# Kernel tuning notes

Measured on AMD Instinct MI355X. Metric: run time of the kernel, lower is better.

## Reference

```python
import jax, jax.numpy as jnp
import numpy as np

B, T, C, H = 2, 2048, 1024, 16
HD = C // H          # head_dim = 64
HALF = HD // 2       # rope half dim = 32
ROPE_BASE = 10000.0


def _build_sin_cos(seq_len, half_dim, base=ROPE_BASE):
    # mirrors build_sin_cos: angles[t, i] = t * base^(-2i / (2*half_dim))
    pos = jnp.arange(seq_len, dtype=jnp.float32)[:, None]                     # [T,1]
    inv_freq = 1.0 / (base ** (jnp.arange(0, half_dim * 2, 2, dtype=jnp.float32) / (half_dim * 2)))
    angles = pos * inv_freq                                                   # [T, half]
    return jnp.sin(angles), jnp.cos(angles)


def setup_inputs() -> dict:
    key = jax.random.key(0)
    k1, k2, k3 = jax.random.split(key, 3)
    x = jax.random.normal(k1, (B, T, C), dtype=jnp.float32)
    # nn.Linear weights (stored as [out,in] in torch; we keep [in,out] for x @ W)
    Wqkv = jax.random.normal(k2, (C, 3 * C), dtype=jnp.float32) * (C ** -0.5)
    Wproj = jax.random.normal(k3, (C, C), dtype=jnp.float32) * (C ** -0.5)
    rope_sin, rope_cos = _build_sin_cos(T, HALF)
    return {"x": x, "Wqkv": Wqkv, "Wproj": Wproj, "rope_sin": rope_sin, "rope_cos": rope_cos}


def reference(x, Wqkv, Wproj, rope_sin, rope_cos):
    Bb, Tt, Cc = x.shape
    Hh = H
    hd = Cc // Hh
    # fused QKV projection, then per-head split (matches view(B,T,H,3*hd).split)
    qkv = (x @ Wqkv).reshape(Bb, Tt, Hh, 3 * hd)
    q, k, v = jnp.split(qkv, 3, axis=-1)                                      # each [B,T,H,hd]
    # RoPE (single device path: local slice == full range)
    s = rope_sin[:Tt][None, :, None, :].astype(x.dtype)                       # [1,T,1,half]
    c = rope_cos[:Tt][None, :, None, :].astype(x.dtype)

    def rot(t):
        t1, t2 = jnp.split(t, 2, axis=-1)
        return jnp.concatenate([t1 * c - t2 * s, t1 * s + t2 * c], axis=-1)

    q = rot(q)
    k = rot(k)
    # causal scaled dot-product attention (flash_attn default scale = hd^-0.5)
    scale = jnp.asarray(hd, x.dtype) ** -0.5
    scores = jnp.einsum('bqhd,bkhd->bhqk', q, k) * scale                      # [B,H,T,T]
    causal = jnp.tril(jnp.ones((Tt, Tt), dtype=bool))
    scores = jnp.where(causal, scores, jnp.finfo(x.dtype).min)
    probs = jax.nn.softmax(scores, axis=-1)
    attn = jnp.einsum('bhqk,bkhd->bqhd', probs, v).reshape(Bb, Tt, Cc)
    return attn @ Wproj
```

## Files before the change

### kernel.cpp

```cpp
#include <hip/hip_runtime.h>

#define Bb 2
#define Tt 2048
#define Cc_ 1024
#define Hh 16
#define HDd 64

typedef __attribute__((ext_vector_type(8))) short bf16x8;
typedef __attribute__((ext_vector_type(4))) float f32x4;
typedef __attribute__((ext_vector_type(4))) unsigned short u16x4;

__device__ __forceinline__ unsigned short f2bf(float f) {
  union { float f; unsigned int u; } v; v.f = f;
  unsigned int r = v.u + 0x7FFFu + ((v.u >> 16) & 1u);
  return (unsigned short)(r >> 16);
}
__device__ __forceinline__ float bf2f(unsigned short u) {
  union { unsigned int u; float f; } v; v.u = ((unsigned int)u) << 16;
  return v.f;
}
__device__ __forceinline__ f32x4 mfma16(bf16x8 a, bf16x8 b, f32x4 c) {
  return __builtin_amdgcn_mfma_f32_16x16x32_bf16(a, b, c, 0, 0, 0);
}
__device__ __forceinline__ void gl_lds16(const void* g, void* l) {
  auto* gp = reinterpret_cast<const __attribute__((address_space(1))) unsigned int*>(
      reinterpret_cast<unsigned long long>(g));
  auto* lp = reinterpret_cast<__attribute__((address_space(3))) unsigned int*>(
      reinterpret_cast<unsigned long long>(l));
  __builtin_amdgcn_global_load_lds(gp, lp, 16, 0, 0);
}

__global__ __launch_bounds__(256) void k_cvt(const float* __restrict__ in,
                                             unsigned short* __restrict__ out, int n4) {
  const int i = blockIdx.x * 256 + threadIdx.x;
  if (i >= n4) return;
  f32x4 v = ((const f32x4*)in)[i];
  u16x4 o;
  o[0] = f2bf(v[0]); o[1] = f2bf(v[1]); o[2] = f2bf(v[2]); o[3] = f2bf(v[3]);
  ((u16x4*)out)[i] = o;
}

__global__ __launch_bounds__(256) void k_tcvt(const float* __restrict__ in,
                                              unsigned short* __restrict__ out, int R, int Cc) {
  __shared__ float tile[32][33];
  const int c0 = blockIdx.x * 32, r0 = blockIdx.y * 32;
  const int tx = threadIdx.x, ty = threadIdx.y;
#pragma unroll
  for (int i = 0; i < 4; ++i)
    tile[ty + i * 8][tx] = in[(size_t)(r0 + ty + i * 8) * Cc + c0 + tx];
  __syncthreads();
#pragma unroll
  for (int i = 0; i < 4; ++i)
    out[(size_t)(c0 + ty + i * 8) * R + r0 + tx] = f2bf(tile[tx][ty + i * 8]);
}

template <bool OUT_BF16>
__global__ __launch_bounds__(256) void k_gemm(const unsigned short* __restrict__ A,
                                              const unsigned short* __restrict__ Bt,
                                              void* __restrict__ Cout, int M, int N, int K) {
  __shared__ unsigned short lA[128 * 64];
  __shared__ unsigned short lB[128 * 64];
  const int tid = threadIdx.x;
  const int lane = tid & 63, wid = tid >> 6;
  const int wr = wid >> 1, wc = wid & 1;
  const int bm = blockIdx.y * 128, bn = blockIdx.x * 128;
  const int l15 = lane & 15, l4 = lane >> 4;
  f32x4 acc[4][4];
#pragma unroll
  for (int i = 0; i < 4; ++i)
#pragma unroll
    for (int j = 0; j < 4; ++j) acc[i][j] = f32x4{0.f, 0.f, 0.f, 0.f};
  const int nk = K >> 6;
  for (int t = 0; t < nk; ++t) {
    const int k0 = t << 6;
    __syncthreads();
#pragma unroll
    for (int i = 0; i < 4; ++i) {
      const int slot = i * 256 + tid;
      const int row = slot >> 3, g = slot & 7;
      const int gs = (g ^ (row & 7)) * 8;
      gl_lds16(A + (size_t)(bm + row) * K + k0 + gs, &lA[slot * 8]);
      gl_lds16(Bt + (size_t)(bn + row) * K + k0 + gs, &lB[slot * 8]);
    }
    __syncthreads();
#pragma unroll
    for (int ks = 0; ks < 2; ++ks) {
      bf16x8 af[4], bfr[4];
#pragma unroll
      for (int mf = 0; mf < 4; ++mf) {
        const int row = wr * 64 + mf * 16 + l15;
        const int g = ks * 4 + l4;
        af[mf] = *(const bf16x8*)&lA[row * 64 + ((g ^ (row & 7)) * 8)];
      }
#pragma unroll
      for (int nf = 0; nf < 4; ++nf) {
        const int row = wc * 64 + nf * 16 + l15;
        const int g = ks * 4 + l4;
        bfr[nf] = *(const bf16x8*)&lB[row * 64 + ((g ^ (row & 7)) * 8)];
      }
#pragma unroll
      for (int mf = 0; mf < 4; ++mf)
#pragma unroll
        for (int nf = 0; nf < 4; ++nf)
          acc[mf][nf] = mfma16(af[mf], bfr[nf], acc[mf][nf]);
    }
  }
  const int rb = bm + wr * 64 + l4 * 4;
  const int cb = bn + wc * 64 + l15;
#pragma unroll
  for (int mf = 0; mf < 4; ++mf)
#pragma unroll
    for (int nf = 0; nf < 4; ++nf)
#pragma unroll
      for (int j = 0; j < 4; ++j) {
        const size_t idx = (size_t)(rb + mf * 16 + j) * N + cb + nf * 16;
        if (OUT_BF16)
          ((unsigned short*)Cout)[idx] = f2bf(acc[mf][nf][j]);
        else
          ((float*)Cout)[idx] = acc[mf][nf][j];
      }
}

__global__ __launch_bounds__(256) void k_rope(const unsigned short* __restrict__ qkv,
                                              const float* __restrict__ rsin,
                                              const float* __restrict__ rcos,
                                              unsigned short* __restrict__ Q,
                                              unsigned short* __restrict__ K) {
  const int tid = blockIdx.x * 256 + threadIdx.x;
  const int d = tid & 31;
  const int t = (tid >> 5) & 2047;
  const int h = (tid >> 16) & 15;
  const int b = tid >> 20;
  const size_t rq = (size_t)(b * Tt + t) * 3072 + h * 192;
  const float q1 = bf2f(qkv[rq + d]), q2 = bf2f(qkv[rq + 32 + d]);
  const float k1 = bf2f(qkv[rq + 64 + d]), k2 = bf2f(qkv[rq + 96 + d]);
  const float s = rsin[t * 32 + d], c = rcos[t * 32 + d];
  const size_t ob = ((size_t)(b * Hh + h) * Tt + t) * 64 + d;
  Q[ob] = f2bf((q1 * c - q2 * s) * 0.125f);
  Q[ob + 32] = f2bf((q1 * s + q2 * c) * 0.125f);
  K[ob] = f2bf(k1 * c - k2 * s);
  K[ob + 32] = f2bf(k1 * s + k2 * c);
}

__global__ __launch_bounds__(256) void k_vrep(const unsigned short* __restrict__ qkv,
                                              unsigned short* __restrict__ Vt) {
  __shared__ unsigned short tile[32][72];
  const int bh = blockIdx.y;
  const int t0 = blockIdx.x * 32;
  const int tx = threadIdx.x, ty = threadIdx.y;
  const int b = bh >> 4, h = bh & 15;
#pragma unroll
  for (int i = 0; i < 4; ++i) {
    const int trow = ty + i * 8;
    const size_t r = (size_t)(b * Tt + t0 + trow) * 3072 + h * 192 + 128;
    tile[trow][tx] = qkv[r + tx];
    tile[trow][tx + 32] = qkv[r + 32 + tx];
  }
  __syncthreads();
#pragma unroll
  for (int i = 0; i < 8; ++i) {
    const int d = ty + i * 8;
    Vt[((size_t)bh * 64 + d) * Tt + t0 + tx] = tile[tx][d];
  }
}

__global__ __launch_bounds__(256) void k_attn(const unsigned short* __restrict__ Q,
                                              const unsigned short* __restrict__ Kt,
                                              const unsigned short* __restrict__ Vt,
                                              unsigned short* __restrict__ Aout) {
  __shared__ unsigned short lK[64 * 64];
  __shared__ unsigned short lV[64 * 64];
  __shared__ unsigned short lP[4][16 * 64];
  const int bxq = blockIdx.x, bh = blockIdx.y;
  const int b = bh >> 4, h = bh & 15;
  const int tid = threadIdx.x, lane = tid & 63, w = tid >> 6;
  const int l15 = lane & 15, l4 = lane >> 4;
  const unsigned short* Kbh = Kt + (size_t)bh * Tt * 64;
  const unsigned short* Vbh = Vt + (size_t)bh * 64 * Tt;
  unsigned short* lPw = lP[w];
  for (int ph = 0; ph < 2; ++ph) {
    const int qt = ph ? bxq : (31 - bxq);
    const int qb = qt * 64;
    const size_t qoff = ((size_t)bh * Tt + qb + w * 16 + l15) * 64 + l4 * 8;
    const bf16x8 qf0 = *(const bf16x8*)&Q[qoff];
    const bf16x8 qf1 = *(const bf16x8*)&Q[qoff + 32];
    f32x4 o[4];
#pragma unroll
    for (int i = 0; i < 4; ++i) o[i] = f32x4{0.f, 0.f, 0.f, 0.f};
    float mrun = -1e30f, lrun = 0.f;
    const int nt = qt + 1;
    for (int t = 0; t < nt; ++t) {
      const int kv0 = t * 64;
      __syncthreads();
#pragma unroll
      for (int i = 0; i < 2; ++i) {
        const int slot = i * 256 + tid;
        const int row = slot >> 3, g = slot & 7;
        const int gs = (g ^ (row & 7)) * 8;
        gl_lds16(Kbh + (size_t)(kv0 + row) * 64 + gs, &lK[slot * 8]);
        gl_lds16(Vbh + (size_t)row * Tt + kv0 + gs, &lV[slot * 8]);
      }
      __syncthreads();
      f32x4 s[4];
#pragma unroll
      for (int i = 0; i < 4; ++i) s[i] = f32x4{0.f, 0.f, 0.f, 0.f};
      __builtin_amdgcn_s_setprio(1);
#pragma unroll
      for (int ks = 0; ks < 2; ++ks) {
        const bf16x8 qa = ks ? qf1 : qf0;
#pragma unroll
        for (int nf = 0; nf < 4; ++nf) {
          const int row = nf * 16 + l15;
          const int g = ks * 4 + l4;
          const bf16x8 kf = *(const bf16x8*)&lK[row * 64 + ((g ^ (row & 7)) * 8)];
          s[nf] = mfma16(kf, qa, s[nf]);
        }
      }
      __builtin_amdgcn_s_setprio(0);
      if (kv0 == qb) {
#pragma unroll
        for (int nf = 0; nf < 4; ++nf)
#pragma unroll
          for (int j = 0; j < 4; ++j)
            if (nf * 16 + l4 * 4 + j > w * 16 + l15) s[nf][j] = -3e38f;
      }
      float mx = s[0][0];
#pragma unroll
      for (int nf = 0; nf < 4; ++nf)
#pragma unroll
        for (int j = 0; j < 4; ++j)
          if (nf | j) mx = fmaxf(mx, s[nf][j]);
      mx = fmaxf(mx, __shfl_xor(mx, 16, 64));
      mx = fmaxf(mx, __shfl_xor(mx, 32, 64));
      const bool need = !__all(mx - mrun <= 8.0f);
      float mnew = mrun;
      if (need) mnew = fmaxf(mrun, mx);
      float ssum = 0.f;
#pragma unroll
      for (int nf = 0; nf < 4; ++nf) {
        u16x4 pk;
#pragma unroll
        for (int j = 0; j < 4; ++j) {
          const float p = __expf(s[nf][j] - mnew);
          ssum += p;
          pk[j] = f2bf(p);
        }
        const int g0 = nf * 2 + (l4 >> 1);
        *(u16x4*)&lPw[l15 * 64 + ((g0 ^ (l15 & 7)) * 8) + (l4 & 1) * 4] = pk;
      }
      ssum += __shfl_xor(ssum, 16, 64);
      ssum += __shfl_xor(ssum, 32, 64);
      if (need) {
        const float alpha = __expf(mrun - mnew);
        lrun = lrun * alpha + ssum;
        mrun = mnew;
        float aj[4];
#pragma unroll
        for (int j = 0; j < 4; ++j) aj[j] = __shfl(alpha, l4 * 4 + j, 64);
#pragma unroll
        for (int df = 0; df < 4; ++df)
#pragma unroll
          for (int j = 0; j < 4; ++j) o[df][j] *= aj[j];
      } else {
        lrun += ssum;
      }
      __builtin_amdgcn_s_setprio(1);
#pragma unroll
      for (int kb = 0; kb < 2; ++kb) {
        const bf16x8 pa = *(const bf16x8*)&lPw[l15 * 64 + (((kb * 4 + l4) ^ (l15 & 7)) * 8)];
#pragma unroll
        for (int df = 0; df < 4; ++df) {
          const int row = df * 16 + l15;
          const int g = kb * 4 + l4;
          const bf16x8 vb = *(const bf16x8*)&lV[row * 64 + ((g ^ (row & 7)) * 8)];
          o[df] = mfma16(pa, vb, o[df]);
        }
      }
      __builtin_amdgcn_s_setprio(0);
    }
    const float rinv = 1.f / lrun;
    float lj[4];
#pragma unroll
    for (int j = 0; j < 4; ++j) lj[j] = __shfl(rinv, l4 * 4 + j, 64);
#pragma unroll
    for (int j = 0; j < 4; ++j) {
      const size_t rr = (size_t)(b * Tt + qb + w * 16 + l4 * 4 + j) * 1024 + h * 64 + l15;
#pragma unroll
      for (int df = 0; df < 4; ++df) Aout[rr + df * 16] = f2bf(o[df][j] * lj[j]);
    }
  }
}

extern "C" void kernel_launch(void* const* d_in, const int* in_sizes, int n_in,
                              void* d_out, int out_size, void* d_ws, size_t ws_size,
                              hipStream_t stream) {
  const float* x = (const float*)d_in[0];
  const float* Wqkv = (const float*)d_in[1];
  const float* Wproj = (const float*)d_in[2];
  const float* rsin = (const float*)d_in[3];
  const float* rcos = (const float*)d_in[4];
  float* out = (float*)d_out;
  char* ws = (char*)d_ws;
  unsigned short* xb = (unsigned short*)(ws);
  unsigned short* wqkvt = (unsigned short*)(ws + (size_t)(8 << 20));
  unsigned short* wprot = (unsigned short*)(ws + (size_t)(14 << 20));
  unsigned short* qkv = (unsigned short*)(ws + (size_t)(16 << 20));
  unsigned short* Q = (unsigned short*)(ws + (size_t)(40 << 20));
  unsigned short* K = (unsigned short*)(ws + (size_t)(48 << 20));
  unsigned short* Vt = (unsigned short*)(ws + (size_t)(56 << 20));
  unsigned short* attn = (unsigned short*)(ws + (size_t)(64 << 20));

  k_cvt<<<4096, 256, 0, stream>>>(x, xb, 1048576);
  k_tcvt<<<dim3(96, 32), dim3(32, 8), 0, stream>>>(Wqkv, wqkvt, 1024, 3072);
  k_tcvt<<<dim3(32, 32), dim3(32, 8), 0, stream>>>(Wproj, wprot, 1024, 1024);
  k_gemm<true><<<dim3(24, 32), 256, 0, stream>>>(xb, wqkvt, qkv, 4096, 3072, 1024);
  k_rope<<<8192, 256, 0, stream>>>(qkv, rsin, rcos, Q, K);
  k_vrep<<<dim3(64, 32), dim3(32, 8), 0, stream>>>(qkv, Vt);
  k_attn<<<dim3(16, 32), 256, 0, stream>>>(Q, K, Vt, attn);
  k_gemm<false><<<dim3(8, 32), 256, 0, stream>>>(attn, wprot, out, 4096, 1024, 1024);
}
```

Baseline: 202.8 us.

## Double-buffer attention KV tiles, shrink query tile, add smaller-tile projection GEMM

Attention now uses 32-row query tiles with 128-thread blocks and twice as many blocks. K/V tiles are double-buffered in LDS so the next tile's global loads overlap the current tile's compute. Softmax moves to exp2 by folding log2(e) into the Q scale, and the max reduction becomes a balanced tree. The output projection switches to a new 128x64-tile GEMM that launches more blocks. The cost is more LDS per block, and smaller tiles mean more K/V reloads per query.

Result: no change. 205.3 us (+1.2%).

```diff
diff --git a/kernel.cpp b/kernel.cpp
--- a/kernel.cpp
+++ b/kernel.cpp
@@ -119,6 +119,72 @@
         else
           ((float*)Cout)[idx] = acc[mf][nf][j];
       }
+}
+
+__global__ __launch_bounds__(256) void k_gemm64(const unsigned short* __restrict__ A,
+                                                const unsigned short* __restrict__ Bt,
+                                                float* __restrict__ Cout, int M, int N, int K) {
+  __shared__ unsigned short lA[128 * 64];
+  __shared__ unsigned short lB[64 * 64];
+  const int tid = threadIdx.x;
+  const int lane = tid & 63, w = tid >> 6;
+  const int bm = blockIdx.y * 128, bn = blockIdx.x * 64;
+  const int l15 = lane & 15, l4 = lane >> 4;
+  f32x4 acc[2][4];
+#pragma unroll
+  for (int i = 0; i < 2; ++i)
+#pragma unroll
+    for (int j = 0; j < 4; ++j) acc[i][j] = f32x4{0.f, 0.f, 0.f, 0.f};
+  const int nk = K >> 6;
+  for (int t = 0; t < nk; ++t) {
+    const int k0 = t << 6;
+    __syncthreads();
+#pragma unroll
+    for (int i = 0; i < 4; ++i) {
+      const int slot = i * 256 + tid;
+      const int row = slot >> 3, g = slot & 7;
+      const int gs = (g ^ (row & 7)) * 8;
+      gl_lds16(A + (size_t)(bm + row) * K + k0 + gs, &lA[slot * 8]);
+    }
+#pragma unroll
+    for (int i = 0; i < 2; ++i) {
+      const int slot = i * 256 + tid;
+      const int row = slot >> 3, g = slot & 7;
+      const int gs = (g ^ (row & 7)) * 8;
+      gl_lds16(Bt + (size_t)(bn + row) * K + k0 + gs, &lB[slot * 8]);
+    }
+    __syncthreads();
+#pragma unroll
+    for (int ks = 0; ks < 2; ++ks) {
+      bf16x8 af[2], bfr[4];
+#pragma unroll
+      for (int mf = 0; mf < 2; ++mf) {
+        const int row = w * 32 + mf * 16 + l15;
+        const int g = ks * 4 + l4;
+        af[mf] = *(const bf16x8*)&lA[row * 64 + ((g ^ (row & 7)) * 8)];
+      }
+#pragma unroll
+      for (int nf = 0; nf < 4; ++nf) {
+        const int row = nf * 16 + l15;
+        const int g = ks * 4 + l4;
+        bfr[nf] = *(const bf16x8*)&lB[row * 64 + ((g ^ (row & 7)) * 8)];
+      }
+#pragma unroll
+      for (int mf = 0; mf < 2; ++mf)
+#pragma unroll
+        for (int nf = 0; nf < 4; ++nf)
+          acc[mf][nf] = mfma16(af[mf], bfr[nf], acc[mf][nf]);
+    }
+  }
+  const int rb = bm + w * 32 + l4 * 4;
+  const int cb = bn + l15;
+#pragma unroll
+  for (int mf = 0; mf < 2; ++mf)
+#pragma unroll
+    for (int nf = 0; nf < 4; ++nf)
+#pragma unroll
+      for (int j = 0; j < 4; ++j)
+        Cout[(size_t)(rb + mf * 16 + j) * N + cb + nf * 16] = acc[mf][nf][j];
 }
 
 __global__ __launch_bounds__(256) void k_rope(const unsigned short* __restrict__ qkv,
@@ -136,8 +202,9 @@
   const float k1 = bf2f(qkv[rq + 64 + d]), k2 = bf2f(qkv[rq + 96 + d]);
   const float s = rsin[t * 32 + d], c = rcos[t * 32 + d];
   const size_t ob = ((size_t)(b * Hh + h) * Tt + t) * 64 + d;
-  Q[ob] = f2bf((q1 * c - q2 * s) * 0.125f);
-  Q[ob + 32] = f2bf((q1 * s + q2 * c) * 0.125f);
+  const float qs = 0.125f * 1.44269504088896f;
+  Q[ob] = f2bf((q1 * c - q2 * s) * qs);
+  Q[ob + 32] = f2bf((q1 * s + q2 * c) * qs);
   K[ob] = f2bf(k1 * c - k2 * s);
   K[ob + 32] = f2bf(k1 * s + k2 * c);
 }
@@ -164,13 +231,13 @@
   }
 }
 
-__global__ __launch_bounds__(256) void k_attn(const unsigned short* __restrict__ Q,
+__global__ __launch_bounds__(128) void k_attn(const unsigned short* __restrict__ Q,
                                               const unsigned short* __restrict__ Kt,
                                               const unsigned short* __restrict__ Vt,
                                               unsigned short* __restrict__ Aout) {
-  __shared__ unsigned short lK[64 * 64];
-  __shared__ unsigned short lV[64 * 64];
-  __shared__ unsigned short lP[4][16 * 64];
+  __shared__ unsigned short lK[2][64 * 64];
+  __shared__ unsigned short lV[2][64 * 64];
+  __shared__ unsigned short lP[2][16 * 64];
   const int bxq = blockIdx.x, bh = blockIdx.y;
   const int b = bh >> 4, h = bh & 15;
   const int tid = threadIdx.x, lane = tid & 63, w = tid >> 6;
@@ -178,9 +245,22 @@
   const unsigned short* Kbh = Kt + (size_t)bh * Tt * 64;
   const unsigned short* Vbh = Vt + (size_t)bh * 64 * Tt;
   unsigned short* lPw = lP[w];
+
+#define STAGE(buf, tt)                                                     \
+  {                                                                        \
+    const int kv0s = (tt) * 64;                                            \
+    _Pragma("unroll") for (int i = 0; i < 4; ++i) {                        \
+      const int slot = i * 128 + tid;                                      \
+      const int row = slot >> 3, g = slot & 7;                             \
+      const int gs = (g ^ (row & 7)) * 8;                                  \
+      gl_lds16(Kbh + (size_t)(kv0s + row) * 64 + gs, &lK[buf][slot * 8]);  \
+      gl_lds16(Vbh + (size_t)row * Tt + kv0s + gs, &lV[buf][slot * 8]);    \
+    }                                                                      \
+  }
+
   for (int ph = 0; ph < 2; ++ph) {
-    const int qt = ph ? bxq : (31 - bxq);
-    const int qb = qt * 64;
+    const int qt = ph ? bxq : (63 - bxq);
+    const int qb = qt * 32;
     const size_t qoff = ((size_t)bh * Tt + qb + w * 16 + l15) * 64 + l4 * 8;
     const bf16x8 qf0 = *(const bf16x8*)&Q[qoff];
     const bf16x8 qf1 = *(const bf16x8*)&Q[qoff + 32];
@@ -188,19 +268,15 @@
 #pragma unroll
     for (int i = 0; i < 4; ++i) o[i] = f32x4{0.f, 0.f, 0.f, 0.f};
     float mrun = -1e30f, lrun = 0.f;
-    const int nt = qt + 1;
+    const int nt = (qt >> 1) + 1;
+    STAGE(0, 0);
+    asm volatile("s_waitcnt vmcnt(0)" ::: "memory");
+    __builtin_amdgcn_s_barrier();
     for (int t = 0; t < nt; ++t) {
+      const int cur = t & 1;
+      const bool more = (t + 1 < nt);
+      if (more) STAGE(cur ^ 1, t + 1);
       const int kv0 = t * 64;
-      __syncthreads();
-#pragma unroll
-      for (int i = 0; i < 2; ++i) {
-        const int slot = i * 256 + tid;
-        const int row = slot >> 3, g = slot & 7;
-        const int gs = (g ^ (row & 7)) * 8;
-        gl_lds16(Kbh + (size_t)(kv0 + row) * 64 + gs, &lK[slot * 8]);
-        gl_lds16(Vbh + (size_t)row * Tt + kv0 + gs, &lV[slot * 8]);
-      }
-      __syncthreads();
       f32x4 s[4];
 #pragma unroll
       for (int i = 0; i < 4; ++i) s[i] = f32x4{0.f, 0.f, 0.f, 0.f};
@@ -212,24 +288,22 @@
         for (int nf = 0; nf < 4; ++nf) {
           const int row = nf * 16 + l15;
           const int g = ks * 4 + l4;
-          const bf16x8 kf = *(const bf16x8*)&lK[row * 64 + ((g ^ (row & 7)) * 8)];
+          const bf16x8 kf = *(const bf16x8*)&lK[cur][row * 64 + ((g ^ (row & 7)) * 8)];
           s[nf] = mfma16(kf, qa, s[nf]);
         }
       }
       __builtin_amdgcn_s_setprio(0);
-      if (kv0 == qb) {
+      if (t == nt - 1) {
 #pragma unroll
         for (int nf = 0; nf < 4; ++nf)
 #pragma unroll
           for (int j = 0; j < 4; ++j)
-            if (nf * 16 + l4 * 4 + j > w * 16 + l15) s[nf][j] = -3e38f;
-      }
-      float mx = s[0][0];
-#pragma unroll
-      for (int nf = 0; nf < 4; ++nf)
-#pragma unroll
-        for (int j = 0; j < 4; ++j)
-          if (nf | j) mx = fmaxf(mx, s[nf][j]);
+            if (kv0 + nf * 16 + l4 * 4 + j > qb + w * 16 + l15) s[nf][j] = -3e38f;
+      }
+      float mx = fmaxf(fmaxf(fmaxf(s[0][0], s[0][1]), fmaxf(s[0][2], s[0][3])),
+                       fmaxf(fmaxf(s[1][0], s[1][1]), fmaxf(s[1][2], s[1][3])));
+      mx = fmaxf(mx, fmaxf(fmaxf(fmaxf(s[2][0], s[2][1]), fmaxf(s[2][2], s[2][3])),
+                           fmaxf(fmaxf(s[3][0], s[3][1]), fmaxf(s[3][2], s[3][3]))));
       mx = fmaxf(mx, __shfl_xor(mx, 16, 64));
       mx = fmaxf(mx, __shfl_xor(mx, 32, 64));
       const bool need = !__all(mx - mrun <= 8.0f);
@@ -241,7 +315,7 @@
         u16x4 pk;
 #pragma unroll
         for (int j = 0; j < 4; ++j) {
-          const float p = __expf(s[nf][j] - mnew);
+          const float p = exp2f(s[nf][j] - mnew);
           ssum += p;
           pk[j] = f2bf(p);
         }
@@ -251,7 +325,7 @@
       ssum += __shfl_xor(ssum, 16, 64);
       ssum += __shfl_xor(ssum, 32, 64);
       if (need) {
-        const float alpha = __expf(mrun - mnew);
+        const float alpha = exp2f(mrun - mnew);
         lrun = lrun * alpha + ssum;
         mrun = mnew;
         float aj[4];
@@ -272,11 +346,13 @@
         for (int df = 0; df < 4; ++df) {
           const int row = df * 16 + l15;
           const int g = kb * 4 + l4;
-          const bf16x8 vb = *(const bf16x8*)&lV[row * 64 + ((g ^ (row & 7)) * 8)];
+          const bf16x8 vb = *(const bf16x8*)&lV[cur][row * 64 + ((g ^ (row & 7)) * 8)];
           o[df] = mfma16(pa, vb, o[df]);
         }
       }
       __builtin_amdgcn_s_setprio(0);
+      if (more) asm volatile("s_waitcnt vmcnt(0)" ::: "memory");
+      __builtin_amdgcn_s_barrier();
     }
     const float rinv = 1.f / lrun;
     float lj[4];
@@ -289,6 +365,7 @@
       for (int df = 0; df < 4; ++df) Aout[rr + df * 16] = f2bf(o[df][j] * lj[j]);
     }
   }
+#undef STAGE
 }
 
 extern "C" void kernel_launch(void* const* d_in, const int* in_sizes, int n_in,
@@ -316,6 +393,6 @@
   k_gemm<true><<<dim3(24, 32), 256, 0, stream>>>(xb, wqkvt, qkv, 4096, 3072, 1024);
   k_rope<<<8192, 256, 0, stream>>>(qkv, rsin, rcos, Q, K);
   k_vrep<<<dim3(64, 32), dim3(32, 8), 0, stream>>>(qkv, Vt);
-  k_attn<<<dim3(16, 32), 256, 0, stream>>>(Q, K, Vt, attn);
-  k_gemm<false><<<dim3(8, 32), 256, 0, stream>>>(attn, wprot, out, 4096, 1024, 1024);
-}
+  k_attn<<<dim3(32, 32), 128, 0, stream>>>(Q, K, Vt, attn);
+  k_gemm64<<<dim3(16, 32), 256, 0, stream>>>(attn, wprot, out, 4096, 1024, 1024);
+}
```
